# Kernel tuning notes

Hardware: AMD Instinct MI355X
Metric: run time of the kernel (lower is better)

## Reference

```python
import jax, jax.numpy as jnp
import numpy as np

B, S, IN_F, OUT_F = 8, 2048, 2048, 2048
ORDER, RANK, LEAF = 3, 4, 13  # LEAF = ceil(IN_F ** (1/ORDER))


def setup_inputs() -> dict:
    key = jax.random.key(0)
    k1, k2, k3, k4 = jax.random.split(key, 4)
    inp = jax.random.normal(k1, (B, S, IN_F), dtype=jnp.float32)
    # leaf init ~ uniform(-std, std), std = gain / in_features**(1/order)
    gain = float(np.sqrt(2.0 / (1.0 + 5.0)))  # leaky_relu gain with param=sqrt(5)
    std = gain / (IN_F ** (1.0 / ORDER))
    leaf_tensor = jax.random.uniform(k2, (ORDER, RANK, LEAF, LEAF), dtype=jnp.float32,
                                     minval=-std, maxval=std)
    bound = 1.0 / np.sqrt(IN_F)
    weight = jax.random.uniform(k3, (OUT_F, IN_F), dtype=jnp.float32, minval=-bound, maxval=bound)
    bias = jax.random.uniform(k4, (OUT_F,), dtype=jnp.float32, minval=-bound, maxval=bound)
    return {"input": inp, "leaf_tensor": leaf_tensor, "weight": weight, "bias": bias}


def tensor_product_represent(leaf_tensor, out_dim, in_dim):
    order, rank, leaf, _ = leaf_tensor.shape  # static shapes
    base = leaf_tensor[0]                      # [rank, leaf, leaf]
    dim = leaf
    for i in range(1, order):                  # fixed small structural loop
        # Kronecker step: [r, d, d] x [r, l, l] -> [r, d*l, d*l]
        base = jnp.einsum('abc,ade->abdce', base, leaf_tensor[i])
        dim = dim * leaf
        base = base.reshape(rank, dim, dim)
    base = base.sum(axis=0)                    # [leaf^order, leaf^order]
    return base[:out_dim, :in_dim]


def reference(input, leaf_tensor, weight, bias):
    out_dim, in_dim = weight.shape
    delta = tensor_product_represent(leaf_tensor, out_dim, in_dim)
    w = weight + delta                          # [out, in]
    # F.linear: y = x @ w.T + b
    return jnp.einsum('bsi,oi->bso', input, w) + bias
```

## Files before the change

### kernel.cpp

```cpp
#include <hip/hip_runtime.h>
#include <hip/hip_bf16.h>
#include <stdint.h>

#define MROWS 16384
#define KDIM  2048
#define NDIM  2048
#define LEAFD 13
#define RANKD 4

typedef __bf16 bf16x8 __attribute__((ext_vector_type(8)));
typedef float  f32x4  __attribute__((ext_vector_type(4)));

__global__ void build_w_kernel(const float* __restrict__ weight,
                               const float* __restrict__ leaf,
                               __hip_bfloat16* __restrict__ wbf) {
    __shared__ float ll[3 * RANKD * LEAFD * LEAFD];
    for (int t = threadIdx.x; t < 3 * RANKD * LEAFD * LEAFD; t += blockDim.x)
        ll[t] = leaf[t];
    __syncthreads();
    int idx = blockIdx.x * blockDim.x + threadIdx.x;
    if (idx >= NDIM * KDIM) return;
    int o = idx / KDIM, i = idx % KDIM;
    int o2 = o / 169, o1 = (o / 13) % 13, o0 = o % 13;
    int i2 = i / 169, i1 = (i / 13) % 13, i0 = i % 13;
    float d = 0.f;
#pragma unroll
    for (int r = 0; r < RANKD; ++r) {
        float a = ll[( r            * LEAFD + o2) * LEAFD + i2];
        float b = ll[((RANKD   + r) * LEAFD + o1) * LEAFD + i1];
        float c = ll[((2*RANKD + r) * LEAFD + o0) * LEAFD + i0];
        d += a * b * c;
    }
    wbf[idx] = __float2bfloat16(weight[idx] + d);
}

__global__ void cvt_kernel(const float* __restrict__ x,
                           __hip_bfloat16* __restrict__ xb, int n) {
    long stride = (long)gridDim.x * blockDim.x * 8;
    for (long idx = ((long)blockIdx.x * blockDim.x + threadIdx.x) * 8; idx < n; idx += stride) {
        float4 v0 = *reinterpret_cast<const float4*>(x + idx);
        float4 v1 = *reinterpret_cast<const float4*>(x + idx + 4);
        __hip_bfloat16 tmp[8];
        tmp[0] = __float2bfloat16(v0.x); tmp[1] = __float2bfloat16(v0.y);
        tmp[2] = __float2bfloat16(v0.z); tmp[3] = __float2bfloat16(v0.w);
        tmp[4] = __float2bfloat16(v1.x); tmp[5] = __float2bfloat16(v1.y);
        tmp[6] = __float2bfloat16(v1.z); tmp[7] = __float2bfloat16(v1.w);
        *reinterpret_cast<uint4*>(xb + idx) = *reinterpret_cast<const uint4*>(tmp);
    }
}


__device__ __forceinline__ void gload16(const __hip_bfloat16* g, char* l) {
    __builtin_amdgcn_global_load_lds((const __attribute__((address_space(1))) void*)g,
                                     (__attribute__((address_space(3))) void*)l,
                                     16, 0, 0);
}

#define STAGE_A(kt, h, BUF) do {                                                        \
    gload16(Abase + (size_t)((h)*128)*KDIM + (kt)*64 + gOff0,                           \
            smemc + (BUF)*65536 + (h)*16384 + sOff0);                                   \
    gload16(Abase + (size_t)((h)*128)*KDIM + (kt)*64 + gOff1,                           \
            smemc + (BUF)*65536 + (h)*16384 + sOff1);                                   \
} while (0)
#define STAGE_B(kt, h, BUF) do {                                                        \
    gload16(Bbase + (size_t)((h)*128)*KDIM + (kt)*64 + gOff0,                           \
            smemc + (BUF)*65536 + 32768 + (h)*16384 + sOff0);                           \
    gload16(Bbase + (size_t)((h)*128)*KDIM + (kt)*64 + gOff1,                           \
            smemc + (BUF)*65536 + 32768 + (h)*16384 + sOff1);                           \
} while (0)

#define RD(off) (*(const bf16x8*)(smemc + (off)))

#define RD_A(BUF, qm) do {                                                              \
    a00 = RD((BUF)*65536 + (qm)*8192 + offA0);                                          \
    a01 = RD((BUF)*65536 + (qm)*8192 + (offA0 ^ 64));                                   \
    a10 = RD((BUF)*65536 + (qm)*8192 + offA1);                                          \
    a11 = RD((BUF)*65536 + (qm)*8192 + (offA1 ^ 64));                                   \
    a20 = RD((BUF)*65536 + (qm)*8192 + offA2);                                          \
    a21 = RD((BUF)*65536 + (qm)*8192 + (offA2 ^ 64));                                   \
    a30 = RD((BUF)*65536 + (qm)*8192 + offA3);                                          \
    a31 = RD((BUF)*65536 + (qm)*8192 + (offA3 ^ 64));                                   \
} while (0)

#define RD_B0(BUF) do {                                                                 \
    b000 = RD((BUF)*65536 + offB0);       b001 = RD((BUF)*65536 + (offB0 ^ 64));        \
    b010 = RD((BUF)*65536 + offB1);       b011 = RD((BUF)*65536 + (offB1 ^ 64));        \
} while (0)
#define RD_B1(BUF) do {                                                                 \
    b100 = RD((BUF)*65536 + 4096 + offB0); b101 = RD((BUF)*65536 + 4096 + (offB0 ^ 64)); \
    b110 = RD((BUF)*65536 + 4096 + offB1); b111 = RD((BUF)*65536 + 4096 + (offB1 ^ 64)); \
} while (0)

#define MFMA_QD(qm, B00,B01,B10,B11, N0, N1) do {                                               \
    acc[(qm)*4+0][N0] = __builtin_amdgcn_mfma_f32_16x16x32_bf16(a00, B00, acc[(qm)*4+0][N0],0,0,0); \
    acc[(qm)*4+1][N0] = __builtin_amdgcn_mfma_f32_16x16x32_bf16(a10, B00, acc[(qm)*4+1][N0],0,0,0); \
    acc[(qm)*4+2][N0] = __builtin_amdgcn_mfma_f32_16x16x32_bf16(a20, B00, acc[(qm)*4+2][N0],0,0,0); \
    acc[(qm)*4+3][N0] = __builtin_amdgcn_mfma_f32_16x16x32_bf16(a30, B00, acc[(qm)*4+3][N0],0,0,0); \
    acc[(qm)*4+0][N1] = __builtin_amdgcn_mfma_f32_16x16x32_bf16(a00, B10, acc[(qm)*4+0][N1],0,0,0); \
    acc[(qm)*4+1][N1] = __builtin_amdgcn_mfma_f32_16x16x32_bf16(a10, B10, acc[(qm)*4+1][N1],0,0,0); \
    acc[(qm)*4+2][N1] = __builtin_amdgcn_mfma_f32_16x16x32_bf16(a20, B10, acc[(qm)*4+2][N1],0,0,0); \
    acc[(qm)*4+3][N1] = __builtin_amdgcn_mfma_f32_16x16x32_bf16(a30, B10, acc[(qm)*4+3][N1],0,0,0); \
    acc[(qm)*4+0][N0] = __builtin_amdgcn_mfma_f32_16x16x32_bf16(a01, B01, acc[(qm)*4+0][N0],0,0,0); \
    acc[(qm)*4+1][N0] = __builtin_amdgcn_mfma_f32_16x16x32_bf16(a11, B01, acc[(qm)*4+1][N0],0,0,0); \
    acc[(qm)*4+2][N0] = __builtin_amdgcn_mfma_f32_16x16x32_bf16(a21, B01, acc[(qm)*4+2][N0],0,0,0); \
    acc[(qm)*4+3][N0] = __builtin_amdgcn_mfma_f32_16x16x32_bf16(a31, B01, acc[(qm)*4+3][N0],0,0,0); \
    acc[(qm)*4+0][N1] = __builtin_amdgcn_mfma_f32_16x16x32_bf16(a01, B11, acc[(qm)*4+0][N1],0,0,0); \
    acc[(qm)*4+1][N1] = __builtin_amdgcn_mfma_f32_16x16x32_bf16(a11, B11, acc[(qm)*4+1][N1],0,0,0); \
    acc[(qm)*4+2][N1] = __builtin_amdgcn_mfma_f32_16x16x32_bf16(a21, B11, acc[(qm)*4+2][N1],0,0,0); \
    acc[(qm)*4+3][N1] = __builtin_amdgcn_mfma_f32_16x16x32_bf16(a31, B11, acc[(qm)*4+3][N1],0,0,0); \
} while (0)

#define BARRIER_IN do {                                     \
    __builtin_amdgcn_sched_barrier(0);                      \
    __builtin_amdgcn_s_barrier();                           \
    asm volatile("s_waitcnt lgkmcnt(0)" ::: "memory");      \
    __builtin_amdgcn_sched_barrier(0);                      \
    __builtin_amdgcn_s_setprio(1);                          \
} while (0)

#define BARRIER_OUT do {                                    \
    __builtin_amdgcn_s_setprio(0);                          \
    __builtin_amdgcn_sched_barrier(0);                      \
    __builtin_amdgcn_s_barrier();                           \
    __builtin_amdgcn_sched_barrier(0);                      \
} while (0)

#define WAIT8 asm volatile("s_waitcnt vmcnt(8)" ::: "memory")
#define WAIT4 asm volatile("s_waitcnt vmcnt(4)" ::: "memory")
#define WAIT0 asm volatile("s_waitcnt vmcnt(0)" ::: "memory")
#define WNONE do {} while (0)

#define KITER(T, S12, SMID, S78, F4_, F8_) do {                     \
                                            \
    RD_A(0, 0); RD_B0(0);                                           \
    if (S12) STAGE_A((T)+1, 0, 1);                                  \
    BARRIER_IN; MFMA_QD(0, b000,b001,b010,b011, 0,1); BARRIER_OUT;  \
                                                 \
    RD_B1(0);                                                       \
    if (S12) STAGE_A((T)+1, 1, 1);                                  \
    BARRIER_IN; MFMA_QD(0, b100,b101,b110,b111, 2,3); BARRIER_OUT;  \
                                                 \
    RD_A(0, 1);                                                     \
    if (SMID) STAGE_B((T)+2, 0, 0);                                 \
    BARRIER_IN; MFMA_QD(1, b000,b001,b010,b011, 0,1); BARRIER_OUT;  \
                                    \
    if (SMID) STAGE_B((T)+2, 1, 0);                                 \
    F4_;                                                            \
    BARRIER_IN; MFMA_QD(1, b100,b101,b110,b111, 2,3); BARRIER_OUT;  \
                                          \
    RD_A(1, 0); RD_B0(1);                                           \
    if (SMID) STAGE_A((T)+2, 0, 0);                                 \
    BARRIER_IN; MFMA_QD(0, b000,b001,b010,b011, 0,1); BARRIER_OUT;  \
                                                 \
    RD_B1(1);                                                       \
    if (SMID) STAGE_A((T)+2, 1, 0);                                 \
    BARRIER_IN; MFMA_QD(0, b100,b101,b110,b111, 2,3); BARRIER_OUT;  \
                                                 \
    RD_A(1, 1);                                                     \
    if (S78) STAGE_B((T)+3, 0, 1);                                  \
    BARRIER_IN; MFMA_QD(1, b000,b001,b010,b011, 0,1); BARRIER_OUT;  \
                                    \
    if (S78) STAGE_B((T)+3, 1, 1);                                  \
    F8_;                                                            \
    BARRIER_IN; MFMA_QD(1, b100,b101,b110,b111, 2,3); BARRIER_OUT;  \
} while (0)

__global__ __launch_bounds__(512, 1) void gemm8p_kernel(const __hip_bfloat16* __restrict__ A,
                                                        const __hip_bfloat16* __restrict__ Wb,
                                                        const float* __restrict__ bias,
                                                        float* __restrict__ C) {
    __shared__ __align__(16) char smem_raw[2 * 65536];
    char* smemc = smem_raw;

    const int tid  = threadIdx.x;
    const int lane = tid & 63;
    const int wid  = tid >> 6;
    const int wr   = wid >> 2;
    const int wc   = wid & 3;

    const int bid = blockIdx.x;
    const int swz = (bid & 7) * 64 + (bid >> 3);
    const int bn  = swz >> 6;
    const int bm  = swz & 63;

    const __hip_bfloat16* Abase = A  + (size_t)bm * 256 * KDIM;
    const __hip_bfloat16* Bbase = Wb + (size_t)bn * 256 * KDIM;

    int gOff0, gOff1;
    {
        const int c0 = wid * 128 + lane;
        const int c1 = c0 + 64;
        const int s0 = c0 ^ ((c0 >> 3) & 7);
        const int s1 = c1 ^ ((c1 >> 3) & 7);
        gOff0 = (s0 >> 3) * KDIM + (s0 & 7) * 8;
        gOff1 = (s1 >> 3) * KDIM + (s1 & 7) * 8;
    }
    const int sOff0 = wid * 2048;
    const int sOff1 = wid * 2048 + 1024;

    const int rsel = lane & 15;
    const int kq   = lane >> 4;
    int offA0, offA1, offA2, offA3, offB0, offB1;
    {
        const int abase = wr * 16384;
#pragma unroll
        for (int mf = 0; mf < 4; ++mf) {
            const int row = mf * 16 + rsel;
            const int off = abase + row * 128 + (kq ^ (row & 7)) * 16;
            if (mf == 0) offA0 = off; else if (mf == 1) offA1 = off;
            else if (mf == 2) offA2 = off; else offA3 = off;
        }
        const int bbase = 32768 + (wc >> 1) * 16384;
#pragma unroll
        for (int nf = 0; nf < 2; ++nf) {
            const int row = (wc & 1) * 64 + nf * 16 + rsel;
            const int off = bbase + row * 128 + (kq ^ (row & 7)) * 16;
            if (nf == 0) offB0 = off; else offB1 = off;
        }
    }

    f32x4 acc[8][4];
#pragma unroll
    for (int m = 0; m < 8; ++m)
#pragma unroll
        for (int n = 0; n < 4; ++n)
            acc[m][n] = (f32x4){0.f, 0.f, 0.f, 0.f};

    bf16x8 a00, a01, a10, a11, a20, a21, a30, a31;
    bf16x8 b000, b001, b010, b011, b100, b101, b110, b111;

    STAGE_A(0, 0, 0); STAGE_A(0, 1, 0); STAGE_B(0, 0, 0); STAGE_B(0, 1, 0);
    STAGE_A(1, 0, 1); STAGE_A(1, 1, 1); STAGE_B(1, 0, 1); STAGE_B(1, 1, 1);
    WAIT8;
    __builtin_amdgcn_sched_barrier(0);
    __builtin_amdgcn_s_barrier();
    __builtin_amdgcn_sched_barrier(0);

    KITER(0, 0, 1, 1, WAIT4, WAIT4);
    for (int i = 1; i < 15; ++i) {
        KITER(2 * i, 1, 1, 1, WAIT4, WAIT4);
    }
    KITER(30, 1, 0, 0, WAIT0, WNONE);

    const int col0 = rsel;
    const int r0   = kq * 4;
#pragma unroll
    for (int n = 0; n < 4; ++n) {
        const int cg = bn * 256 + wc * 64 + n * 16 + col0;
        const float bv = bias[cg];
#pragma unroll
        for (int m = 0; m < 8; ++m) {
            const size_t rg = (size_t)bm * 256 + wr * 128 + m * 16 + r0;
#pragma unroll
            for (int r = 0; r < 4; ++r)
                C[(rg + r) * NDIM + cg] = acc[m][n][r] + bv;
        }
    }
}

__global__ void naive_kernel(const float* __restrict__ x,
                             const float* __restrict__ leaf,
                             const float* __restrict__ W,
                             const float* __restrict__ bias,
                             float* __restrict__ out) {
    long idx = (long)blockIdx.x * blockDim.x + threadIdx.x;
    if (idx >= (long)MROWS * NDIM) return;
    int  o = (int)(idx % NDIM);
    long m = idx / NDIM;
    int o2 = o / 169, o1 = (o / 13) % 13, o0 = o % 13;
    float acc = 0.f;
    for (int i = 0; i < KDIM; ++i) {
        int i2 = i / 169, i1 = (i / 13) % 13, i0 = i % 13;
        float d = 0.f;
#pragma unroll
        for (int r = 0; r < RANKD; ++r)
            d += leaf[( r     * LEAFD + o2) * LEAFD + i2]
               * leaf[((4 + r) * LEAFD + o1) * LEAFD + i1]
               * leaf[((8 + r) * LEAFD + o0) * LEAFD + i0];
        acc += x[m * KDIM + i] * (W[(long)o * KDIM + i] + d);
    }
    out[idx] = acc + bias[o];
}

extern "C" void kernel_launch(void* const* d_in, const int* in_sizes, int n_in,
                              void* d_out, int out_size, void* d_ws, size_t ws_size,
                              hipStream_t stream) {
    const float* x      = (const float*)d_in[0];
    const float* leaf   = (const float*)d_in[1];
    const float* weight = (const float*)d_in[2];
    const float* bias   = (const float*)d_in[3];
    float* out = (float*)d_out;

    const size_t needA = (size_t)MROWS * KDIM * sizeof(__hip_bfloat16);
    const size_t needW = (size_t)NDIM  * KDIM * sizeof(__hip_bfloat16);

    if (ws_size >= needA + needW) {
        __hip_bfloat16* xb = (__hip_bfloat16*)d_ws;
        __hip_bfloat16* wb = (__hip_bfloat16*)((char*)d_ws + needA);
        build_w_kernel<<<(NDIM * KDIM + 255) / 256, 256, 0, stream>>>(weight, leaf, wb);
        cvt_kernel<<<2048, 256, 0, stream>>>(x, xb, MROWS * KDIM);
        gemm8p_kernel<<<(MROWS / 256) * (NDIM / 256), 512, 0, stream>>>(xb, wb, bias, out);
    } else {
        long total = (long)MROWS * NDIM;
        naive_kernel<<<(int)((total + 255) / 256), 256, 0, stream>>>(x, leaf, weight, bias, out);
    }
}
```

Measured before the change: 209.2 us.

## Rework GEMM main loop to single barrier per phase with prefetched B fragments

```diff
diff --git a/kernel.cpp b/kernel.cpp
--- a/kernel.cpp
+++ b/kernel.cpp
@@ -82,13 +82,17 @@
     a31 = RD((BUF)*65536 + (qm)*8192 + (offA3 ^ 64));                                   \
 } while (0)
 
-#define RD_B0(BUF) do {                                                                 \
-    b000 = RD((BUF)*65536 + offB0);       b001 = RD((BUF)*65536 + (offB0 ^ 64));        \
-    b010 = RD((BUF)*65536 + offB1);       b011 = RD((BUF)*65536 + (offB1 ^ 64));        \
+#define RD_B0Y(BUF) do {                                                                \
+    by00 = RD((BUF)*65536 + offB0);        by01 = RD((BUF)*65536 + (offB0 ^ 64));       \
+    by10 = RD((BUF)*65536 + offB1);        by11 = RD((BUF)*65536 + (offB1 ^ 64));       \
+} while (0)
+#define RD_B0X(BUF) do {                                                                \
+    bx00 = RD((BUF)*65536 + offB0);        bx01 = RD((BUF)*65536 + (offB0 ^ 64));       \
+    bx10 = RD((BUF)*65536 + offB1);        bx11 = RD((BUF)*65536 + (offB1 ^ 64));       \
 } while (0)
 #define RD_B1(BUF) do {                                                                 \
-    b100 = RD((BUF)*65536 + 4096 + offB0); b101 = RD((BUF)*65536 + 4096 + (offB0 ^ 64)); \
-    b110 = RD((BUF)*65536 + 4096 + offB1); b111 = RD((BUF)*65536 + 4096 + (offB1 ^ 64)); \
+    bq00 = RD((BUF)*65536 + 4096 + offB0); bq01 = RD((BUF)*65536 + 4096 + (offB0 ^ 64)); \
+    bq10 = RD((BUF)*65536 + 4096 + offB1); bq11 = RD((BUF)*65536 + 4096 + (offB1 ^ 64)); \
 } while (0)
 
 #define MFMA_QD(qm, B00,B01,B10,B11, N0, N1) do {                                               \
@@ -110,65 +114,61 @@
     acc[(qm)*4+3][N1] = __builtin_amdgcn_mfma_f32_16x16x32_bf16(a31, B11, acc[(qm)*4+3][N1],0,0,0); \
 } while (0)
 
-#define BARRIER_IN do {                                     \
-    __builtin_amdgcn_sched_barrier(0);                      \
-    __builtin_amdgcn_s_barrier();                           \
-    asm volatile("s_waitcnt lgkmcnt(0)" ::: "memory");      \
-    __builtin_amdgcn_sched_barrier(0);                      \
-    __builtin_amdgcn_s_setprio(1);                          \
-} while (0)
-
-#define BARRIER_OUT do {                                    \
-    __builtin_amdgcn_s_setprio(0);                          \
-    __builtin_amdgcn_sched_barrier(0);                      \
-    __builtin_amdgcn_s_barrier();                           \
-    __builtin_amdgcn_sched_barrier(0);                      \
-} while (0)
-
-#define WAIT8 asm volatile("s_waitcnt vmcnt(8)" ::: "memory")
-#define WAIT4 asm volatile("s_waitcnt vmcnt(4)" ::: "memory")
-#define WAIT0 asm volatile("s_waitcnt vmcnt(0)" ::: "memory")
-#define WNONE do {} while (0)
-
-#define KITER(T, S12, SMID, S78, F4_, F8_) do {                     \
-                                            \
-    RD_A(0, 0); RD_B0(0);                                           \
-    if (S12) STAGE_A((T)+1, 0, 1);                                  \
-    BARRIER_IN; MFMA_QD(0, b000,b001,b010,b011, 0,1); BARRIER_OUT;  \
-                                                 \
+#define BAR __builtin_amdgcn_s_barrier()
+#define F2  asm volatile("s_waitcnt vmcnt(2)" ::: "memory")
+#define FD0 asm volatile("s_waitcnt vmcnt(0)" ::: "memory")
+#define FW8 asm volatile("s_waitcnt vmcnt(8)" ::: "memory")
+#define FNONE do {} while (0)
+
+#define KITER(T, PS1, PS23, PS45, PS67, PS8, F4_, F8_, RP8) do {    \
+                                                            \
+    RD_A(0, 0);                                                     \
+    if (PS1)  STAGE_B((T)+1, 1, 1);                                 \
+    BAR;                                                            \
+    MFMA_QD(0, by00,by01,by10,by11, 0,1);                           \
+                                                            \
     RD_B1(0);                                                       \
-    if (S12) STAGE_A((T)+1, 1, 1);                                  \
-    BARRIER_IN; MFMA_QD(0, b100,b101,b110,b111, 2,3); BARRIER_OUT;  \
-                                                 \
+    if (PS23) STAGE_A((T)+1, 0, 1);                                 \
+    BAR;                                                            \
+    MFMA_QD(0, bq00,bq01,bq10,bq11, 2,3);                           \
+                                                            \
     RD_A(0, 1);                                                     \
-    if (SMID) STAGE_B((T)+2, 0, 0);                                 \
-    BARRIER_IN; MFMA_QD(1, b000,b001,b010,b011, 0,1); BARRIER_OUT;  \
-                                    \
-    if (SMID) STAGE_B((T)+2, 1, 0);                                 \
+    if (PS23) STAGE_A((T)+1, 1, 1);                                 \
+    BAR;                                                            \
+    MFMA_QD(1, by00,by01,by10,by11, 0,1);                           \
+                                                            \
+    if (PS45) STAGE_B((T)+2, 0, 0);                                 \
     F4_;                                                            \
-    BARRIER_IN; MFMA_QD(1, b100,b101,b110,b111, 2,3); BARRIER_OUT;  \
-                                          \
-    RD_A(1, 0); RD_B0(1);                                           \
-    if (SMID) STAGE_A((T)+2, 0, 0);                                 \
-    BARRIER_IN; MFMA_QD(0, b000,b001,b010,b011, 0,1); BARRIER_OUT;  \
-                                                 \
+    RD_B0X(1);                                                      \
+    BAR;                                                            \
+    MFMA_QD(1, bq00,bq01,bq10,bq11, 2,3);                           \
+                                                            \
+    RD_A(1, 0);                                                     \
+    if (PS45) STAGE_B((T)+2, 1, 0);                                 \
+    BAR;                                                            \
+    MFMA_QD(0, bx00,bx01,bx10,bx11, 0,1);                           \
+                                                            \
     RD_B1(1);                                                       \
-    if (SMID) STAGE_A((T)+2, 1, 0);                                 \
-    BARRIER_IN; MFMA_QD(0, b100,b101,b110,b111, 2,3); BARRIER_OUT;  \
-                                                 \
+    if (PS67) STAGE_A((T)+2, 0, 0);                                 \
+    BAR;                                                            \
+    MFMA_QD(0, bq00,bq01,bq10,bq11, 2,3);                           \
+                                                            \
     RD_A(1, 1);                                                     \
-    if (S78) STAGE_B((T)+3, 0, 1);                                  \
-    BARRIER_IN; MFMA_QD(1, b000,b001,b010,b011, 0,1); BARRIER_OUT;  \
-                                    \
-    if (S78) STAGE_B((T)+3, 1, 1);                                  \
+    if (PS67) STAGE_A((T)+2, 1, 0);                                 \
+    BAR;                                                            \
+    MFMA_QD(1, bx00,bx01,bx10,bx11, 0,1);                           \
+                                                            \
+    if (PS8)  STAGE_B((T)+3, 0, 1);                                 \
     F8_;                                                            \
-    BARRIER_IN; MFMA_QD(1, b100,b101,b110,b111, 2,3); BARRIER_OUT;  \
-} while (0)
-
-__global__ __launch_bounds__(512, 1) void gemm8p_kernel(const __hip_bfloat16* __restrict__ A,
-                                                        const __hip_bfloat16* __restrict__ Wb,
-                                                        const float* __restrict__ bias,
-                                                        float* __restrict__ C) {
+    if (RP8)  RD_B0Y(0);                                            \
+    BAR;                                                            \
+    MFMA_QD(1, bq00,bq01,bq10,bq11, 2,3);                           \
+} while (0)
+
+__global__ __launch_bounds__(512, 1) void gemm9_kernel(const __hip_bfloat16* __restrict__ A,
+                                                       const __hip_bfloat16* __restrict__ Wb,
+                                                       const float* __restrict__ bias,
+                                                       float* __restrict__ C) {
     __shared__ __align__(16) char smem_raw[2 * 65536];
     char* smemc = smem_raw;
 
@@ -227,20 +227,21 @@
             acc[m][n] = (f32x4){0.f, 0.f, 0.f, 0.f};
 
     bf16x8 a00, a01, a10, a11, a20, a21, a30, a31;
-    bf16x8 b000, b001, b010, b011, b100, b101, b110, b111;
+    bf16x8 by00, by01, by10, by11;
+    bf16x8 bx00, bx01, bx10, bx11;
+    bf16x8 bq00, bq01, bq10, bq11;
 
     STAGE_A(0, 0, 0); STAGE_A(0, 1, 0); STAGE_B(0, 0, 0); STAGE_B(0, 1, 0);
     STAGE_A(1, 0, 1); STAGE_A(1, 1, 1); STAGE_B(1, 0, 1); STAGE_B(1, 1, 1);
-    WAIT8;
-    __builtin_amdgcn_sched_barrier(0);
-    __builtin_amdgcn_s_barrier();
-    __builtin_amdgcn_sched_barrier(0);
-
-    KITER(0, 0, 1, 1, WAIT4, WAIT4);
+    FW8;
+    BAR;
+    RD_B0Y(0);
+
+    KITER(0, 0, 0, 1, 1, 1, F2, F2, 1);
     for (int i = 1; i < 15; ++i) {
-        KITER(2 * i, 1, 1, 1, WAIT4, WAIT4);
-    }
-    KITER(30, 1, 0, 0, WAIT0, WNONE);
+        KITER(2 * i, 1, 1, 1, 1, 1, F2, F2, 1);
+    }
+    KITER(30, 1, 1, 0, 0, 0, FD0, FNONE, 0);
 
     const int col0 = rsel;
     const int r0   = kq * 4;
@@ -299,7 +300,7 @@
         __hip_bfloat16* wb = (__hip_bfloat16*)((char*)d_ws + needA);
         build_w_kernel<<<(NDIM * KDIM + 255) / 256, 256, 0, stream>>>(weight, leaf, wb);
         cvt_kernel<<<2048, 256, 0, stream>>>(x, xb, MROWS * KDIM);
-        gemm8p_kernel<<<(MROWS / 256) * (NDIM / 256), 512, 0, stream>>>(xb, wb, bias, out);
+        gemm9_kernel<<<(MROWS / 256) * (NDIM / 256), 512, 0, stream>>>(xb, wb, bias, out);
     } else {
         long total = (long)MROWS * NDIM;
         naive_kernel<<<(int)((total + 255) / 256), 256, 0, stream>>>(x, leaf, weight, bias, out);
```

Result: no change. 211.4 us (+1.0%).
